# Kernel optimization log

Hardware: AMD Instinct MI355X
Metric: run time of the kernel (lower is better)

The kernel has to match this reference:

```python
import jax, jax.numpy as jnp
import numpy as np

N_RAYS = 8192
N_SURF = 2048
EPS = 1e-18  # matches torch zero-denominator patch value


def setup_inputs() -> dict:
    key = jax.random.key(0)
    k1, k2, k3 = jax.random.split(key, 3)
    o = jax.random.normal(k1, (N_RAYS, 3), dtype=jnp.float32)
    d = jax.random.normal(k2, (N_RAYS, 3), dtype=jnp.float32)
    V = jax.random.normal(k3, (N_SURF, 4, 3), dtype=jnp.float32)
    return {"o": o, "d": d, "V": V}


def _safe(x):
    # torch code sets exact-zero denominators to 1e-18 via nonzero() indexing
    return jnp.where(x == 0.0, EPS, x)


def reference(o, d, V):
    # --- get_intersections: ray-plane intersection scalars t (N, M) ---
    v = jnp.cross(V[:, 1] - V[:, 0], V[:, 2] - V[:, 0])          # (M,3) plane normals
    v = v / jnp.linalg.norm(v, axis=1, keepdims=True)
    k = -jnp.sum(v * V[:, 3], axis=1)                             # (M,) plane offsets
    vo = o @ v.T                                                  # (N,M)
    vd = d @ v.T                                                  # (N,M)
    t = -(k[None, :] + vo) / vd                                   # (N,M)

    # intersection points r = o + t*d, broadcast over surfaces -> (N,M,3)
    r = o[:, None, :] + t[..., None] * d[:, None, :]

    # --- get_onsurface_surface_intersections: barycentric masking ---
    a = V[None, :, 0]  # (1,M,3) broadcast instead of .repeat
    b = V[None, :, 1]
    c = V[None, :, 2]
    ax, ay, az = a[..., 0], a[..., 1], a[..., 2]
    rx, ry, rz = r[..., 0], r[..., 1], r[..., 2]

    A = ax * rz - az * rx
    B = ax * b[..., 2] - az * b[..., 0]
    C = ax * ry - ay * rx
    D = ax * b[..., 1] - ay * b[..., 0]
    E = ax * c[..., 2] - az * c[..., 0]
    F = B * (ay * c[..., 0] - ax * c[..., 1])
    G = D

    gam = (G * (A * D - B * C)) / _safe(D * (E * G + F))          # (N,M)
    beta = (C + gam * (ay * c[..., 0] - ax * c[..., 1])) / _safe(D)
    alpha = (rx - (beta * b[..., 0] + gam * c[..., 0])) / _safe(ax)

    mask = (beta > 0.0) & (gam > 0.0) & (alpha > 0.0)             # (N,M) bool
    return t * mask.astype(t.dtype)                               # masked intersection depths
```

## Files before the change

kernel.cpp:

```cpp
#include <hip/hip_runtime.h>


#define N_RAYS 8192
#define N_SURF 2048
constexpr int RPB = 32;

__device__ __forceinline__ float safef(float x) {
    return (x == 0.0f) ? 1e-18f : x;
}

__global__ __launch_bounds__(256, 8) void trace_kernel(
    const float* __restrict__ o, const float* __restrict__ dr,
    const float* __restrict__ V, float* __restrict__ out)
{
    const int s = blockIdx.x * 256 + threadIdx.x;

    const float4 p0 = *(const float4*)(V + (size_t)s * 12);
    const float4 p1 = *(const float4*)(V + (size_t)s * 12 + 4);
    const float4 p2 = *(const float4*)(V + (size_t)s * 12 + 8);
    const float ax = p0.x, ay = p0.y, az = p0.z;
    const float bx = p0.w, by = p1.x, bz = p1.y;
    const float cx = p1.z, cy = p1.w, cz = p2.x;
    const float wx = p2.y, wy = p2.z, wz = p2.w;

    const float e0x = bx - ax, e0y = by - ay, e0z = bz - az;
    const float e1x = cx - ax, e1y = cy - ay, e1z = cz - az;
    const float nx = e0y * e1z - e0z * e1y;
    const float ny = e0z * e1x - e0x * e1z;
    const float nz = e0x * e1y - e0y * e1x;
    const float rn = __builtin_amdgcn_rsqf(fmaf(nx, nx, fmaf(ny, ny, nz * nz)));
    const float vx = nx * rn, vy = ny * rn, vz = nz * rn;
    const float k = -fmaf(vx, wx, fmaf(vy, wy, vz * wz));

    const float B  = ax * bz - az * bx;
    const float D  = ax * by - ay * bx;
    const float E  = ax * cz - az * cx;
    const float P  = ay * cx - ax * cy;
    const float F  = B * P;
    const float rden = __builtin_amdgcn_rcpf(safef(D * fmaf(E, D, F)));
    const float rD   = __builtin_amdgcn_rcpf(safef(D));
    const float rAX  = __builtin_amdgcn_rcpf(safef(ax));

    const float DB = D * B, DD = D * D;
    const float g0 = (DB * ay - DD * az) * rden;
    const float g1 = -(DB * ax) * rden;
    const float g2 = (DD * ax) * rden;
    const float bp  = P * rD;
    const float bb0 = fmaf(bp, g0, -ay * rD);
    const float bb1 = fmaf(bp, g1,  ax * rD);
    const float bb2 = bp * g2;
    const float ab = -bx * rAX, ac = -cx * rAX;
    const float aa0 = fmaf(ab, bb0, fmaf(ac, g0, rAX));
    const float aa1 = fmaf(ab, bb1, ac * g1);
    const float aa2 = fmaf(ab, bb2, ac * g2);

    const int ray0 = blockIdx.y * RPB;
    float* outp = out + (size_t)ray0 * N_SURF + s;
#pragma unroll 4
    for (int i = 0; i < RPB; ++i) {
        const int ray = ray0 + i;
        const float o0 = o[ray * 3 + 0], o1 = o[ray * 3 + 1], o2 = o[ray * 3 + 2];
        const float d0 = dr[ray * 3 + 0], d1 = dr[ray * 3 + 1], d2 = dr[ray * 3 + 2];

        const float vo_k = fmaf(o0, vx, fmaf(o1, vy, fmaf(o2, vz, k)));
        const float vd   = fmaf(d0, vx, fmaf(d1, vy, d2 * vz));
        const float t    = -vo_k * __builtin_amdgcn_rcpf(vd);

        const float rx = fmaf(t, d0, o0);
        const float ry = fmaf(t, d1, o1);
        const float rz = fmaf(t, d2, o2);

        const float gam   = fmaf(g0,  rx, fmaf(g1,  ry, g2  * rz));
        const float beta  = fmaf(bb0, rx, fmaf(bb1, ry, bb2 * rz));
        const float alpha = fmaf(aa0, rx, fmaf(aa1, ry, aa2 * rz));

        const float mn = fminf(fminf(beta, gam), alpha);
        outp[(size_t)i * N_SURF] = (mn > 0.0f) ? t : 0.0f;
    }
}

extern "C" void kernel_launch(void* const* d_in, const int* in_sizes, int n_in,
                              void* d_out, int out_size, void* d_ws, size_t ws_size,
                              hipStream_t stream) {
    const float* o  = (const float*)d_in[0];
    const float* dr = (const float*)d_in[1];
    const float* V  = (const float*)d_in[2];
    float* out = (float*)d_out;

    trace_kernel<<<dim3(N_SURF / 256, N_RAYS / RPB), dim3(256), 0, stream>>>(o, dr, V, out);
}
```

Before: 84.91 us.

## Precompute per-surface coefficients in separate kernel and vectorize output stores

Moves the per-surface plane and barycentric coefficient setup into a small precompute kernel that writes them to workspace. The trace kernel now has each thread handle 4 consecutive surfaces across all 2048 per block, processing 8 rays per block, and writes results as float4. This is meant to cut the redundant per-block coefficient work and widen the stores, at the cost of an extra launch, a workspace round trip and higher register pressure.

```diff
diff --git a/kernel.cpp b/kernel.cpp
--- a/kernel.cpp
+++ b/kernel.cpp
@@ -3,15 +3,23 @@
 
 #define N_RAYS 8192
 #define N_SURF 2048
-constexpr int RPB = 32;
+constexpr int TPB = 512;
+constexpr int SPT = 4;
+constexpr int RPB = 8;
 
 __device__ __forceinline__ float safef(float x) {
     return (x == 0.0f) ? 1e-18f : x;
 }
 
-__global__ __launch_bounds__(256, 8) void trace_kernel(
-    const float* __restrict__ o, const float* __restrict__ dr,
-    const float* __restrict__ V, float* __restrict__ out)
+struct Coeffs {
+    float vx, vy, vz, k;
+    float g0, g1, g2;
+    float bb0, bb1, bb2;
+    float aa0, aa1, aa2;
+};
+
+__global__ __launch_bounds__(256) void precompute_kernel(
+    const float* __restrict__ V, float* __restrict__ C)
 {
     const int s = blockIdx.x * 256 + threadIdx.x;
 
@@ -45,7 +53,7 @@
     const float g0 = (DB * ay - DD * az) * rden;
     const float g1 = -(DB * ax) * rden;
     const float g2 = (DD * ax) * rden;
-    const float bp  = P * rD;
+    const float bp = P * rD;
     const float bb0 = fmaf(bp, g0, -ay * rD);
     const float bb1 = fmaf(bp, g1,  ax * rD);
     const float bb2 = bp * g2;
@@ -54,28 +62,63 @@
     const float aa1 = fmaf(ab, bb1, ac * g1);
     const float aa2 = fmaf(ab, bb2, ac * g2);
 
-    const int ray0 = blockIdx.y * RPB;
-    float* outp = out + (size_t)ray0 * N_SURF + s;
-#pragma unroll 4
+    float4* c4 = (float4*)(C + (size_t)s * 16);
+    c4[0] = make_float4(vx, vy, vz, k);
+    c4[1] = make_float4(g0, g1, g2, 0.0f);
+    c4[2] = make_float4(bb0, bb1, bb2, 0.0f);
+    c4[3] = make_float4(aa0, aa1, aa2, 0.0f);
+}
+
+__device__ __forceinline__ float trace_pair(
+    const Coeffs& c, float o0, float o1, float o2, float d0, float d1, float d2)
+{
+    const float vo_k = fmaf(o0, c.vx, fmaf(o1, c.vy, fmaf(o2, c.vz, c.k)));
+    const float vd   = fmaf(d0, c.vx, fmaf(d1, c.vy, d2 * c.vz));
+    const float t    = -vo_k * __builtin_amdgcn_rcpf(vd);
+
+    const float rx = fmaf(t, d0, o0);
+    const float ry = fmaf(t, d1, o1);
+    const float rz = fmaf(t, d2, o2);
+
+    const float gam   = fmaf(c.g0,  rx, fmaf(c.g1,  ry, c.g2  * rz));
+    const float beta  = fmaf(c.bb0, rx, fmaf(c.bb1, ry, c.bb2 * rz));
+    const float alpha = fmaf(c.aa0, rx, fmaf(c.aa1, ry, c.aa2 * rz));
+
+    const float mn = fminf(fminf(beta, gam), alpha);
+    return (mn > 0.0f) ? t : 0.0f;
+}
+
+__global__ __launch_bounds__(TPB, 6) void trace_kernel(
+    const float* __restrict__ o, const float* __restrict__ dr,
+    const float* __restrict__ C, float* __restrict__ out)
+{
+    const int s0 = threadIdx.x * SPT;
+
+    Coeffs c[SPT];
+#pragma unroll
+    for (int j = 0; j < SPT; ++j) {
+        const float4* c4 = (const float4*)(C + (size_t)(s0 + j) * 16);
+        const float4 q0 = c4[0], q1 = c4[1], q2 = c4[2], q3 = c4[3];
+        c[j].vx = q0.x; c[j].vy = q0.y; c[j].vz = q0.z; c[j].k = q0.w;
+        c[j].g0 = q1.x; c[j].g1 = q1.y; c[j].g2 = q1.z;
+        c[j].bb0 = q2.x; c[j].bb1 = q2.y; c[j].bb2 = q2.z;
+        c[j].aa0 = q3.x; c[j].aa1 = q3.y; c[j].aa2 = q3.z;
+    }
+
+    const int ray0 = blockIdx.x * RPB;
+    float* outp = out + (size_t)ray0 * N_SURF + s0;
+#pragma unroll 2
     for (int i = 0; i < RPB; ++i) {
         const int ray = ray0 + i;
         const float o0 = o[ray * 3 + 0], o1 = o[ray * 3 + 1], o2 = o[ray * 3 + 2];
         const float d0 = dr[ray * 3 + 0], d1 = dr[ray * 3 + 1], d2 = dr[ray * 3 + 2];
 
-        const float vo_k = fmaf(o0, vx, fmaf(o1, vy, fmaf(o2, vz, k)));
-        const float vd   = fmaf(d0, vx, fmaf(d1, vy, d2 * vz));
-        const float t    = -vo_k * __builtin_amdgcn_rcpf(vd);
+        float res[SPT];
+#pragma unroll
+        for (int j = 0; j < SPT; ++j)
+            res[j] = trace_pair(c[j], o0, o1, o2, d0, d1, d2);
 
-        const float rx = fmaf(t, d0, o0);
-        const float ry = fmaf(t, d1, o1);
-        const float rz = fmaf(t, d2, o2);
-
-        const float gam   = fmaf(g0,  rx, fmaf(g1,  ry, g2  * rz));
-        const float beta  = fmaf(bb0, rx, fmaf(bb1, ry, bb2 * rz));
-        const float alpha = fmaf(aa0, rx, fmaf(aa1, ry, aa2 * rz));
-
-        const float mn = fminf(fminf(beta, gam), alpha);
-        outp[(size_t)i * N_SURF] = (mn > 0.0f) ? t : 0.0f;
+        *(float4*)(outp + (size_t)i * N_SURF) = *(const float4*)res;
     }
 }
 
@@ -86,6 +129,8 @@
     const float* dr = (const float*)d_in[1];
     const float* V  = (const float*)d_in[2];
     float* out = (float*)d_out;
+    float* C = (float*)d_ws;
 
-    trace_kernel<<<dim3(N_SURF / 256, N_RAYS / RPB), dim3(256), 0, stream>>>(o, dr, V, out);
+    precompute_kernel<<<dim3(N_SURF / 256), dim3(256), 0, stream>>>(V, C);
+    trace_kernel<<<dim3(N_RAYS / RPB), dim3(TPB), 0, stream>>>(o, dr, C, out);
 }
```

Measured after the change: 147.6 us. 1.74x slower.
